# Performance work log

Hardware: AMD Instinct MI355X
Metric: run time of the kernel (lower is better)

Reference implementation:

```python
import jax, jax.numpy as jnp
import numpy as np

B, N, M, C, H = 8, 2048, 1024, 512, 8
D = C // H  # per-head dim = 64


def setup_inputs() -> dict:
    key = jax.random.key(0)
    ks = jax.random.split(key, 4)
    x = jax.random.normal(ks[0], (B, N, C), dtype=jnp.float32)
    global_tokens = jax.random.normal(ks[1], (B, M, C), dtype=jnp.float32)
    Wq = jax.random.normal(ks[2], (C, C), dtype=jnp.float32) * 0.02
    bq = jnp.zeros((C,), dtype=jnp.float32)
    Wkv = jax.random.normal(ks[3], (C, 2 * C), dtype=jnp.float32) * 0.02
    bkv = jnp.zeros((2 * C,), dtype=jnp.float32)
    return {"x": x, "global_tokens": global_tokens, "Wq": Wq, "bq": bq,
            "Wkv": Wkv, "bkv": bkv}


def reference(x, global_tokens, Wq, bq, Wkv, bkv):
    # q from x, k/v from global_tokens (LinearProjection with query=True)
    q = (x @ Wq + bq).reshape(B, N, H, D).transpose(0, 2, 1, 3)        # [B,H,N,D]
    kv = (global_tokens @ Wkv + bkv).reshape(B, M, 2, H, D)
    k = kv[:, :, 0].transpose(0, 2, 1, 3)                              # [B,H,M,D]
    v = kv[:, :, 1].transpose(0, 2, 1, 3)                              # [B,H,M,D]
    # NOTE: original module applies no 1/sqrt(D) scaling in forward
    attn = jnp.einsum('bhnd,bhmd->bhnm', q, k)                         # [B,H,N,M]
    attn = jax.nn.softmax(attn, axis=-1)
    out = jnp.einsum('bhnm,bhmd->bhnd', attn, v)                       # [B,H,N,D]
    return out.transpose(0, 2, 1, 3).reshape(B, N, C)
```

## Files before the change

### kernel.cpp

```cpp
#include <hip/hip_runtime.h>
#include <hip/hip_bf16.h>


typedef __bf16 bf16_t;
typedef __bf16 bf16x8 __attribute__((ext_vector_type(8)));
typedef __bf16 bf16x4 __attribute__((ext_vector_type(4)));
typedef float floatx16 __attribute__((ext_vector_type(16)));
typedef unsigned int uintx4 __attribute__((ext_vector_type(4)));
typedef unsigned int uintx2 __attribute__((ext_vector_type(2)));

#define KDIM 512
#define QSCALE 1.44269504088896f

__device__ __forceinline__ unsigned pack2(float a, float b) {
  unsigned short ua = __builtin_bit_cast(unsigned short, (bf16_t)a);
  unsigned short ub = __builtin_bit_cast(unsigned short, (bf16_t)b);
  return (unsigned)ua | ((unsigned)ub << 16);
}

__device__ __forceinline__ float fexp2(float x) {
#if __has_builtin(__builtin_amdgcn_exp2f)
  return __builtin_amdgcn_exp2f(x);
#else
  return __exp2f(x);
#endif
}

__device__ __forceinline__ bf16x8 cvt8(const float4 a, const float4 b) {
  bf16x8 r;
  r[0] = (bf16_t)a.x; r[1] = (bf16_t)a.y; r[2] = (bf16_t)a.z; r[3] = (bf16_t)a.w;
  r[4] = (bf16_t)b.x; r[5] = (bf16_t)b.y; r[6] = (bf16_t)b.z; r[7] = (bf16_t)b.w;
  return r;
}

__device__ __forceinline__ void gl_lds16(const bf16_t* g, bf16_t* l) {
#if __has_builtin(__builtin_amdgcn_global_load_lds)
  __builtin_amdgcn_global_load_lds(
      (const __attribute__((address_space(1))) unsigned int*)(g),
      (__attribute__((address_space(3))) unsigned int*)(l), 16, 0, 0);
#else
  *(bf16x8*)l = *(const bf16x8*)g;
#endif
}

__global__ __launch_bounds__(256) void transpose_cvt_kernel(
    const float* __restrict__ Wq, const float* __restrict__ Wkv,
    bf16_t* __restrict__ Wqt, bf16_t* __restrict__ Wkvt) {
  __shared__ float tile[64][65];
  const int blk = blockIdx.x;
  const float* in; bf16_t* out; int N, bx, by;
  if (blk < 64) { in = Wq; out = Wqt; N = 512; bx = blk & 7; by = blk >> 3; }
  else { int t2 = blk - 64; in = Wkv; out = Wkvt; N = 1024; bx = t2 & 15; by = t2 >> 4; }
  const int t = threadIdx.x;
  const int c0 = bx * 64, k0 = by * 64;
#pragma unroll
  for (int i = 0; i < 16; ++i) {
    int idx = t + i * 256;
    int kk = idx >> 6, cc = idx & 63;
    tile[kk][cc] = in[(size_t)(k0 + kk) * N + (c0 + cc)];
  }
  __syncthreads();
#pragma unroll
  for (int j = 0; j < 2; ++j) {
    int unit = t + j * 256;
    int cc = unit >> 3, ks = (unit & 7) * 8;
    int c = c0 + cc, k = k0 + ks;
    bf16x8 v;
#pragma unroll
    for (int i = 0; i < 8; ++i) v[i] = (bf16_t)tile[ks + i][cc];
    *(bf16x8*)(&out[(size_t)((c >> 7) * 16 + (k >> 5)) * 4096 + (c & 127) * 32 + (k & 31)]) = v;
  }
}

__global__ __launch_bounds__(256) void proj_gemm_kernel(
    const float* __restrict__ x, const float* __restrict__ gt,
    const bf16_t* __restrict__ Wqt, const bf16_t* __restrict__ Wkvt,
    const float* __restrict__ bq, const float* __restrict__ bkv,
    bf16_t* __restrict__ Qf, bf16_t* __restrict__ Kf, bf16_t* __restrict__ Vf) {
  __shared__ bf16_t lA[128 * 40];
  __shared__ bf16_t lW[4096];
  const int blk = blockIdx.x;
  int mode, bx, by;
  const float* A; const bf16_t* Wt; const float* bias;
  if (blk < 512) { mode = 0; bx = blk & 3; by = blk >> 2; A = x; Wt = Wqt; bias = bq; }
  else { int tt = blk - 512; mode = 1; bx = tt & 7; by = tt >> 3; A = gt; Wt = Wkvt; bias = bkv; }

  const int tid = threadIdx.x;
  const int wave = tid >> 6, L = tid & 63;
  const int l5 = L & 31, hf = L >> 5;
  const int wr = wave >> 1, wc = wave & 1;
  const int rb = by * 128, cb = bx * 128;

  floatx16 acc[2][2] = {};

  const int arow = tid >> 1, akq = (tid & 1) * 16;
  const float* Ap = A + (size_t)(rb + arow) * KDIM + akq;
  bf16_t* lAw = &lA[arow * 40 + akq];
  const bf16_t* Wbase = Wt + (size_t)bx * 16 * 4096;

  float4 f0 = *(const float4*)(Ap);
  float4 f1 = *(const float4*)(Ap + 4);
  float4 f2 = *(const float4*)(Ap + 8);
  float4 f3 = *(const float4*)(Ap + 12);

  for (int kt = 0; kt < 16; ++kt) {
    __syncthreads();
#pragma unroll
    for (int j = 0; j < 2; ++j) {
      const int s = wave * 2 + j;
      gl_lds16(Wbase + (size_t)kt * 4096 + s * 512 + L * 8, &lW[s * 512 + L * 8]);
    }
    *(bf16x8*)(lAw) = cvt8(f0, f1);
    *(bf16x8*)(lAw + 8) = cvt8(f2, f3);
    __syncthreads();
    if (kt < 15) {
      Ap += 32;
      f0 = *(const float4*)(Ap);
      f1 = *(const float4*)(Ap + 4);
      f2 = *(const float4*)(Ap + 8);
      f3 = *(const float4*)(Ap + 12);
    }
    bf16x8 af[2][2], wf[2][2];
#pragma unroll
    for (int rs = 0; rs < 2; ++rs)
#pragma unroll
      for (int kh = 0; kh < 2; ++kh)
        af[rs][kh] = *(const bf16x8*)(&lA[(wr * 64 + rs * 32 + l5) * 40 + kh * 16 + hf * 8]);
#pragma unroll
    for (int cs = 0; cs < 2; ++cs)
#pragma unroll
      for (int kh = 0; kh < 2; ++kh)
        wf[cs][kh] = *(const bf16x8*)(&lW[(wc * 64 + cs * 32 + l5) * 32 + kh * 16 + hf * 8]);
#pragma unroll
    for (int rs = 0; rs < 2; ++rs)
#pragma unroll
      for (int cs = 0; cs < 2; ++cs)
#pragma unroll
        for (int kh = 0; kh < 2; ++kh)
          acc[rs][cs] = __builtin_amdgcn_mfma_f32_32x32x16_bf16(
              af[rs][kh], wf[cs][kh], acc[rs][cs], 0, 0, 0);
  }

#pragma unroll
  for (int rs = 0; rs < 2; ++rs)
#pragma unroll
    for (int cs = 0; cs < 2; ++cs) {
      const int col = cb + wc * 64 + cs * 32 + l5;
      const float bv = bias[col];
      const int grb = rb + wr * 64 + rs * 32;
      if (mode == 0) {
        const int hh = col >> 6, d = col & 63;
        const int dof = (d >> 3) * 256 + (d & 7);
#pragma unroll
        for (int r = 0; r < 16; ++r) {
          int gr = grb + (r & 3) + 8 * (r >> 2) + 4 * hf;
          int b = gr >> 11, n = gr & 2047;
          Qf[(size_t)(b * 8 + hh) * 131072 + (n >> 5) * 2048 + dof + (n & 31) * 8] =
              (bf16_t)((acc[rs][cs][r] + bv) * QSCALE);
        }
      } else if (col < 512) {
        const int hh = col >> 6, d = col & 63;
        const int dof = (d >> 3) * 256 + (d & 7);
#pragma unroll
        for (int r = 0; r < 16; ++r) {
          int gr = grb + (r & 3) + 8 * (r >> 2) + 4 * hf;
          int b = gr >> 10, m = gr & 1023;
          Kf[(size_t)(b * 8 + hh) * 65536 + (m >> 5) * 2048 + dof + (m & 31) * 8] =
              (bf16_t)(acc[rs][cs][r] + bv);
        }
      } else {
        const int cc = col - 512;
        const int hh = cc >> 6, d = cc & 63;
        const int dof = (d >> 5) * 1024 + (d & 31) * 8;
#pragma unroll
        for (int rq = 0; rq < 4; ++rq) {
          int gr = grb + 8 * rq + 4 * hf;
          int b = gr >> 10, m = gr & 1023;
          bf16x4 pk;
          pk[0] = (bf16_t)(acc[rs][cs][rq * 4 + 0] + bv);
          pk[1] = (bf16_t)(acc[rs][cs][rq * 4 + 1] + bv);
          pk[2] = (bf16_t)(acc[rs][cs][rq * 4 + 2] + bv);
          pk[3] = (bf16_t)(acc[rs][cs][rq * 4 + 3] + bv);
          *(bf16x4*)(&Vf[(size_t)(b * 8 + hh) * 65536 + (m >> 5) * 2048 + dof +
                         ((m >> 4) & 1) * 512 + ((m >> 3) & 1) * 256 + (m & 7)]) = pk;
        }
      }
    }
}

__global__ __launch_bounds__(256, 4) void flash_attn_kernel(
    const bf16_t* __restrict__ Qf, const bf16_t* __restrict__ Kf,
    const bf16_t* __restrict__ Vf, float* __restrict__ out) {
  __shared__ bf16_t kv[2][2][4096];
  const int tid = threadIdx.x;
  const int wave = tid >> 6, L = tid & 63;
  const int l5 = L & 31, hf = L >> 5;
  const int bh = blockIdx.y;
  const int b = bh >> 3, hh = bh & 7;
  const int nb = blockIdx.x * 128 + wave * 32;

  const bf16_t* Qp = Qf + (size_t)bh * 131072 + (nb >> 5) * 2048 + L * 8;
  const bf16_t* Kb = Kf + (size_t)bh * 65536 + L * 8;
  const bf16_t* Vb = Vf + (size_t)bh * 65536 + L * 8;

  bf16x8 qf[4];
#pragma unroll
  for (int kc = 0; kc < 4; ++kc) qf[kc] = *(const bf16x8*)(Qp + kc * 512);

  bf16x8 ones;
#pragma unroll
  for (int i = 0; i < 8; ++i) ones[i] = (bf16_t)1.0f;

  floatx16 o0 = {}, o1 = {}, lacc = {};

  auto dma = [&](int buf, int ep2) {
#pragma unroll
    for (int j = 0; j < 4; ++j) {
      const int s = wave * 4 + j;
      const int sub = s >> 3, q = s & 7;
      const bf16_t* g = (q < 4) ? (Kb + (size_t)(ep2 * 2 + sub) * 2048 + q * 512)
                                : (Vb + (size_t)(ep2 * 2 + sub) * 2048 + (q - 4) * 512);
      bf16_t* l = &kv[buf][sub][(q < 4 ? q * 512 : 2048 + (q - 4) * 512) + L * 8];
      gl_lds16(g, l);
    }
  };

  dma(0, 0);
  __syncthreads();

  for (int ep = 0; ep < 16; ++ep) {
    const int cur = ep & 1;
    if (ep < 15) dma(cur ^ 1, ep + 1);
#pragma unroll
    for (int sub = 0; sub < 2; ++sub) {
      const bf16_t* kb = &kv[cur][sub][L * 8];
      const bf16_t* vb = &kv[cur][sub][2048 + L * 8];
      bf16x8 kf4[4];
#pragma unroll
      for (int kc = 0; kc < 4; ++kc) kf4[kc] = *(const bf16x8*)(kb + kc * 512);
      floatx16 sa = {};
#pragma unroll
      for (int kc = 0; kc < 4; ++kc)
        sa = __builtin_amdgcn_mfma_f32_32x32x16_bf16(kf4[kc], qf[kc], sa, 0, 0, 0);
      bf16x8 vf4[4];
#pragma unroll
      for (int j = 0; j < 4; ++j) vf4[j] = *(const bf16x8*)(vb + j * 512);
      unsigned w[8];
#pragma unroll
      for (int i = 0; i < 8; ++i) {
        float pa = fexp2(sa[2 * i]), pb = fexp2(sa[2 * i + 1]);
        w[i] = pack2(pa, pb);
      }
      uintx4 fw0, fw1;
#if __has_builtin(__builtin_amdgcn_permlane32_swap)
      {
        uintx2 r0 = __builtin_amdgcn_permlane32_swap(w[0], w[2], false, false);
        uintx2 r1 = __builtin_amdgcn_permlane32_swap(w[1], w[3], false, false);
        uintx2 r2 = __builtin_amdgcn_permlane32_swap(w[4], w[6], false, false);
        uintx2 r3 = __builtin_amdgcn_permlane32_swap(w[5], w[7], false, false);
        fw0.x = r0[0]; fw0.z = r0[1];
        fw0.y = r1[0]; fw0.w = r1[1];
        fw1.x = r2[0]; fw1.z = r2[1];
        fw1.y = r3[0]; fw1.w = r3[1];
      }
#else
      {
        unsigned sw[8];
#pragma unroll
        for (int i = 0; i < 8; ++i) sw[i] = __shfl_xor(w[i], 32);
        fw0.x = hf ? sw[2] : w[0]; fw0.y = hf ? sw[3] : w[1];
        fw0.z = hf ? w[2] : sw[0]; fw0.w = hf ? w[3] : sw[1];
        fw1.x = hf ? sw[6] : w[4]; fw1.y = hf ? sw[7] : w[5];
        fw1.z = hf ? w[6] : sw[4]; fw1.w = hf ? w[7] : sw[5];
      }
#endif
      bf16x8 pf0 = __builtin_bit_cast(bf16x8, fw0);
      bf16x8 pf1 = __builtin_bit_cast(bf16x8, fw1);
      lacc = __builtin_amdgcn_mfma_f32_32x32x16_bf16(ones, pf0, lacc, 0, 0, 0);
      lacc = __builtin_amdgcn_mfma_f32_32x32x16_bf16(ones, pf1, lacc, 0, 0, 0);
      o0 = __builtin_amdgcn_mfma_f32_32x32x16_bf16(vf4[0], pf0, o0, 0, 0, 0);
      o0 = __builtin_amdgcn_mfma_f32_32x32x16_bf16(vf4[1], pf1, o0, 0, 0, 0);
      o1 = __builtin_amdgcn_mfma_f32_32x32x16_bf16(vf4[2], pf0, o1, 0, 0, 0);
      o1 = __builtin_amdgcn_mfma_f32_32x32x16_bf16(vf4[3], pf1, o1, 0, 0, 0);
    }
    __syncthreads();
  }

  const float inv = 1.0f / lacc[0];

  float* lob = (float*)(&kv[0][0][0]) + wave * (32 * 36);
  const size_t orow = (size_t)b * 2048 + nb;
#pragma unroll
  for (int pass = 0; pass < 2; ++pass) {
    const floatx16& oo = pass ? o1 : o0;
#pragma unroll
    for (int i = 0; i < 8; ++i) {
      const int d = 2 * (i & 1) + 8 * (i >> 1) + 4 * hf;
      float2 a;
      a.x = oo[2 * i] * inv; a.y = oo[2 * i + 1] * inv;
      *(float2*)(&lob[l5 * 36 + d]) = a;
    }
#pragma unroll
    for (int j = 0; j < 4; ++j) {
      int chunk = j * 64 + L;
      int n = chunk >> 3, c = chunk & 7;
      float4 v = *(const float4*)(&lob[n * 36 + c * 4]);
      *(float4*)(&out[(orow + n) * 512 + hh * 64 + pass * 32 + c * 4]) = v;
    }
  }
}

extern "C" void kernel_launch(void* const* d_in, const int* in_sizes, int n_in,
                              void* d_out, int out_size, void* d_ws, size_t ws_size,
                              hipStream_t stream) {
  (void)in_sizes; (void)n_in; (void)out_size; (void)ws_size;
  const float* x   = (const float*)d_in[0];
  const float* gt  = (const float*)d_in[1];
  const float* Wq  = (const float*)d_in[2];
  const float* bq  = (const float*)d_in[3];
  const float* Wkv = (const float*)d_in[4];
  const float* bkv = (const float*)d_in[5];
  float* out = (float*)d_out;

  bf16_t* Wqt  = (bf16_t*)d_ws;
  bf16_t* Wkvt = Wqt + (size_t)512 * 512;
  bf16_t* Qf   = Wkvt + (size_t)1024 * 512;
  bf16_t* Kf   = Qf + (size_t)64 * 2048 * 64;
  bf16_t* Vf   = Kf + (size_t)64 * 1024 * 64;

  transpose_cvt_kernel<<<192, 256, 0, stream>>>(Wq, Wkv, Wqt, Wkvt);
  proj_gemm_kernel<<<1024, 256, 0, stream>>>(x, gt, Wqt, Wkvt, bq, bkv, Qf, Kf, Vf);
  flash_attn_kernel<<<dim3(16, 64), 256, 0, stream>>>(Qf, Kf, Vf, out);
}
```

Baseline: 182.9 us.

## Pre-convert activations to bf16 tiled layout and double-buffer projection GEMM via LDS DMA

The prep kernel now also converts x and global_tokens from fp32 to bf16 in a pre-tiled fragment layout, stored temporarily in the output buffer. The projection GEMM loads both A and W tiles straight into LDS with global_load_lds and double-buffers them, so the next k-tile is fetched while the current one is used. The in-loop fp32 load and convert and one barrier per iteration go away. In exchange there is an extra pass that writes and rereads the bf16 activations, and the kernel relies on the output buffer being free until the attention kernel runs.

```diff
diff --git a/kernel.cpp b/kernel.cpp
--- a/kernel.cpp
+++ b/kernel.cpp
@@ -43,47 +43,70 @@
 #endif
 }
 
-__global__ __launch_bounds__(256) void transpose_cvt_kernel(
+__global__ __launch_bounds__(256) void prep_kernel(
     const float* __restrict__ Wq, const float* __restrict__ Wkv,
-    bf16_t* __restrict__ Wqt, bf16_t* __restrict__ Wkvt) {
+    const float* __restrict__ x, const float* __restrict__ gt,
+    bf16_t* __restrict__ Wqt, bf16_t* __restrict__ Wkvt,
+    bf16_t* __restrict__ Aq, bf16_t* __restrict__ Akv) {
   __shared__ float tile[64][65];
   const int blk = blockIdx.x;
-  const float* in; bf16_t* out; int N, bx, by;
-  if (blk < 64) { in = Wq; out = Wqt; N = 512; bx = blk & 7; by = blk >> 3; }
-  else { int t2 = blk - 64; in = Wkv; out = Wkvt; N = 1024; bx = t2 & 15; by = t2 >> 4; }
   const int t = threadIdx.x;
-  const int c0 = bx * 64, k0 = by * 64;
-#pragma unroll
-  for (int i = 0; i < 16; ++i) {
-    int idx = t + i * 256;
-    int kk = idx >> 6, cc = idx & 63;
-    tile[kk][cc] = in[(size_t)(k0 + kk) * N + (c0 + cc)];
+  if (blk < 192) {
+    const float* in; bf16_t* out; int N, bx, by;
+    if (blk < 64) { in = Wq; out = Wqt; N = 512; bx = blk & 7; by = blk >> 3; }
+    else { int t2 = blk - 64; in = Wkv; out = Wkvt; N = 1024; bx = t2 & 15; by = t2 >> 4; }
+    const int c0 = bx * 64, k0 = by * 64;
+#pragma unroll
+    for (int i = 0; i < 16; ++i) {
+      int idx = t + i * 256;
+      int kk = idx >> 6, cc = idx & 63;
+      tile[kk][cc] = in[(size_t)(k0 + kk) * N + (c0 + cc)];
+    }
+    __syncthreads();
+#pragma unroll
+    for (int j = 0; j < 2; ++j) {
+      int unit = t + j * 256;
+      int cc = unit >> 3, ks = (unit & 7) * 8;
+      int c = c0 + cc, k = k0 + ks;
+      bf16x8 v;
+#pragma unroll
+      for (int i = 0; i < 8; ++i) v[i] = (bf16_t)tile[ks + i][cc];
+      const int k5 = k & 31;
+      const int chunk = ((c & 127) >> 5) * 2 + (k5 >> 4);
+      *(bf16x8*)(&out[(size_t)((c >> 7) * 16 + (k >> 5)) * 4096 + chunk * 512 +
+                      (c & 31) * 8 + ((k5 >> 3) & 1) * 256]) = v;
+    }
+  } else {
+    int idx = blk - 192;
+    const float* src; bf16_t* dst; int rt, kt2;
+    if (idx < 2048) { src = x; dst = Aq; rt = idx >> 4; kt2 = idx & 15; }
+    else { int i2 = idx - 2048; src = gt; dst = Akv; rt = i2 >> 4; kt2 = i2 & 15; }
+    const int row = rt * 128 + (t >> 1);
+    const int kb = kt2 * 32 + (t & 1) * 16;
+    const float* p = src + (size_t)row * KDIM + kb;
+    float4 f0 = *(const float4*)(p);
+    float4 f1 = *(const float4*)(p + 4);
+    float4 f2 = *(const float4*)(p + 8);
+    float4 f3 = *(const float4*)(p + 12);
+    bf16x8 o0 = cvt8(f0, f1), o1 = cvt8(f2, f3);
+    const int chunk = ((row & 127) >> 5) * 2 + (t & 1);
+    bf16_t* ob = dst + (size_t)(rt * 16 + kt2) * 4096 + chunk * 512 + (row & 31) * 8;
+    *(bf16x8*)(ob) = o0;
+    *(bf16x8*)(ob + 256) = o1;
   }
-  __syncthreads();
-#pragma unroll
-  for (int j = 0; j < 2; ++j) {
-    int unit = t + j * 256;
-    int cc = unit >> 3, ks = (unit & 7) * 8;
-    int c = c0 + cc, k = k0 + ks;
-    bf16x8 v;
-#pragma unroll
-    for (int i = 0; i < 8; ++i) v[i] = (bf16_t)tile[ks + i][cc];
-    *(bf16x8*)(&out[(size_t)((c >> 7) * 16 + (k >> 5)) * 4096 + (c & 127) * 32 + (k & 31)]) = v;
-  }
 }
 
 __global__ __launch_bounds__(256) void proj_gemm_kernel(
-    const float* __restrict__ x, const float* __restrict__ gt,
+    const bf16_t* __restrict__ Aq, const bf16_t* __restrict__ Akv,
     const bf16_t* __restrict__ Wqt, const bf16_t* __restrict__ Wkvt,
     const float* __restrict__ bq, const float* __restrict__ bkv,
     bf16_t* __restrict__ Qf, bf16_t* __restrict__ Kf, bf16_t* __restrict__ Vf) {
-  __shared__ bf16_t lA[128 * 40];
-  __shared__ bf16_t lW[4096];
+  __shared__ bf16_t lds[2][8192];
   const int blk = blockIdx.x;
   int mode, bx, by;
-  const float* A; const bf16_t* Wt; const float* bias;
-  if (blk < 512) { mode = 0; bx = blk & 3; by = blk >> 2; A = x; Wt = Wqt; bias = bq; }
-  else { int tt = blk - 512; mode = 1; bx = tt & 7; by = tt >> 3; A = gt; Wt = Wkvt; bias = bkv; }
+  const bf16_t* Ab; const bf16_t* Wb; const float* bias;
+  if (blk < 512) { mode = 0; bx = blk & 3; by = blk >> 2; Ab = Aq; Wb = Wqt; bias = bq; }
+  else { int tt = blk - 512; mode = 1; bx = tt & 7; by = tt >> 3; Ab = Akv; Wb = Wkvt; bias = bkv; }
 
   const int tid = threadIdx.x;
   const int wave = tid >> 6, L = tid & 63;
@@ -91,46 +114,37 @@
   const int wr = wave >> 1, wc = wave & 1;
   const int rb = by * 128, cb = bx * 128;
 
+  const bf16_t* Abase = Ab + (size_t)by * 16 * 4096 + L * 8;
+  const bf16_t* Wbase = Wb + (size_t)bx * 16 * 4096 + L * 8;
+
+  auto dma = [&](int buf, int kt) {
+#pragma unroll
+    for (int j = 0; j < 4; ++j) {
+      const int s = wave * 4 + j;
+      const bf16_t* g = (s < 8) ? (Abase + (size_t)kt * 4096 + s * 512)
+                                : (Wbase + (size_t)kt * 4096 + (s - 8) * 512);
+      gl_lds16(g, &lds[buf][(s < 8 ? s * 512 : 4096 + (s - 8) * 512) + L * 8]);
+    }
+  };
+
+  dma(0, 0);
+  __syncthreads();
+
   floatx16 acc[2][2] = {};
-
-  const int arow = tid >> 1, akq = (tid & 1) * 16;
-  const float* Ap = A + (size_t)(rb + arow) * KDIM + akq;
-  bf16_t* lAw = &lA[arow * 40 + akq];
-  const bf16_t* Wbase = Wt + (size_t)bx * 16 * 4096;
-
-  float4 f0 = *(const float4*)(Ap);
-  float4 f1 = *(const float4*)(Ap + 4);
-  float4 f2 = *(const float4*)(Ap + 8);
-  float4 f3 = *(const float4*)(Ap + 12);
-
   for (int kt = 0; kt < 16; ++kt) {
-    __syncthreads();
-#pragma unroll
-    for (int j = 0; j < 2; ++j) {
-      const int s = wave * 2 + j;
-      gl_lds16(Wbase + (size_t)kt * 4096 + s * 512 + L * 8, &lW[s * 512 + L * 8]);
-    }
-    *(bf16x8*)(lAw) = cvt8(f0, f1);
-    *(bf16x8*)(lAw + 8) = cvt8(f2, f3);
-    __syncthreads();
-    if (kt < 15) {
-      Ap += 32;
-      f0 = *(const float4*)(Ap);
-      f1 = *(const float4*)(Ap + 4);
-      f2 = *(const float4*)(Ap + 8);
-      f3 = *(const float4*)(Ap + 12);
-    }
+    const int cur = kt & 1;
+    if (kt < 15) dma(cur ^ 1, kt + 1);
     bf16x8 af[2][2], wf[2][2];
 #pragma unroll
     for (int rs = 0; rs < 2; ++rs)
 #pragma unroll
       for (int kh = 0; kh < 2; ++kh)
-        af[rs][kh] = *(const bf16x8*)(&lA[(wr * 64 + rs * 32 + l5) * 40 + kh * 16 + hf * 8]);
+        af[rs][kh] = *(const bf16x8*)(&lds[cur][((wr * 2 + rs) * 2 + kh) * 512 + L * 8]);
 #pragma unroll
     for (int cs = 0; cs < 2; ++cs)
 #pragma unroll
       for (int kh = 0; kh < 2; ++kh)
-        wf[cs][kh] = *(const bf16x8*)(&lW[(wc * 64 + cs * 32 + l5) * 32 + kh * 16 + hf * 8]);
+        wf[cs][kh] = *(const bf16x8*)(&lds[cur][4096 + ((wc * 2 + cs) * 2 + kh) * 512 + L * 8]);
 #pragma unroll
     for (int rs = 0; rs < 2; ++rs)
 #pragma unroll
@@ -139,6 +153,7 @@
         for (int kh = 0; kh < 2; ++kh)
           acc[rs][cs] = __builtin_amdgcn_mfma_f32_32x32x16_bf16(
               af[rs][kh], wf[cs][kh], acc[rs][cs], 0, 0, 0);
+    __syncthreads();
   }
 
 #pragma unroll
@@ -327,8 +342,10 @@
   bf16_t* Qf   = Wkvt + (size_t)1024 * 512;
   bf16_t* Kf   = Qf + (size_t)64 * 2048 * 64;
   bf16_t* Vf   = Kf + (size_t)64 * 1024 * 64;
-
-  transpose_cvt_kernel<<<192, 256, 0, stream>>>(Wq, Wkv, Wqt, Wkvt);
-  proj_gemm_kernel<<<1024, 256, 0, stream>>>(x, gt, Wqt, Wkvt, bq, bkv, Qf, Kf, Vf);
+  bf16_t* Aq   = (bf16_t*)d_out;
+  bf16_t* Akv  = Aq + (size_t)16384 * 512;
+
+  prep_kernel<<<3264, 256, 0, stream>>>(Wq, Wkv, x, gt, Wqt, Wkvt, Aq, Akv);
+  proj_gemm_kernel<<<1024, 256, 0, stream>>>(Aq, Akv, Wqt, Wkvt, bq, bkv, Qf, Kf, Vf);
   flash_attn_kernel<<<dim3(16, 64), 256, 0, stream>>>(Qf, Kf, Vf, out);
 }
```

Measured after the change: 180.9 us. No clear change (-1.1%).
